# Kernel optimization log

Measured on AMD Instinct MI355X. Metric: run time of the kernel, lower is better.

Reference implementation:

```python
import jax, jax.numpy as jnp
import numpy as np

N = 100_000          # nodes
E = 3_200_000        # edges (avg degree 32)
H = 20               # hidden_channels (node feature width, = 10 one-hot + 10 mlp)
EH = 64              # edge_hidden_dim
EO = 10              # edge_output_dim
THRESHOLD = 1.0


def setup_inputs() -> dict:
    key = jax.random.key(0)
    ks = jax.random.split(key, 12)
    x = jax.random.normal(ks[0], (N, 2, H), dtype=jnp.float32)
    edge_index = jax.random.randint(ks[1], (2, E), 0, N, dtype=jnp.int32)
    # distances strictly in (0, threshold]
    edge_attr = jax.random.uniform(ks[2], (E, 1), jnp.float32, 1e-4, THRESHOLD)
    # parameters (torch.rand init as in the module)
    a = jax.random.uniform(ks[3], (1,), jnp.float32)
    b = jax.random.uniform(ks[4], (1,), jnp.float32) + 1.0
    gamma1 = jax.random.uniform(ks[5], (H, H), jnp.float32)
    gamma2 = jax.random.uniform(ks[6], (H, H), jnp.float32)
    bias = jax.random.uniform(ks[7], (H,), jnp.float32)
    # edge MLP: Linear(1, EH) -> ReLU -> Linear(EH, EO)
    W1 = jax.random.normal(ks[8], (1, EH), jnp.float32)
    b1 = jnp.zeros((EH,), jnp.float32)
    W2 = jax.random.normal(ks[9], (EH, EO), jnp.float32) / np.sqrt(EH)
    b2 = jnp.zeros((EO,), jnp.float32)
    return dict(x=x, edge_index=edge_index, edge_attr=edge_attr, a=a, b=b,
                gamma1=gamma1, gamma2=gamma2, bias=bias, W1=W1, b1=b1, W2=W2, b2=b2)


def reference(x, edge_index, edge_attr, a, b, gamma1, gamma2, bias, W1, b1, W2, b2):
    src, dst = edge_index[0], edge_index[1]
    # --- edge features ---
    h = jax.nn.relu(edge_attr @ W1 + b1)            # [E, EH]
    mlp_out = h @ W2 + b2                           # [E, EO]
    # one-hot distance bucket: 10 equal intervals over (0, threshold], idx 10 -> 9
    idx = jnp.clip((edge_attr[:, 0] * (10.0 / THRESHOLD)).astype(jnp.int32), 0, 9)
    one_hot = jax.nn.one_hot(idx, 10, dtype=x.dtype)  # [E, 10]
    eac = jnp.concatenate([one_hot, mlp_out], axis=1)  # edge_attr_combined [E, 20]
    # --- per-source-node normalization (w_tilde) ---
    sum_w = jax.ops.segment_sum(eac, src, num_segments=N)  # [N, 20]
    sw = sum_w[src]                                        # [E, 20]
    safe = jnp.where(sw != 0, sw, 1.0)
    w_tilde = jnp.where(sw != 0, eac / safe, jnp.asarray(0.01, x.dtype))
    # --- rho weighting on node features ---
    h_j = x[src, 0]                                  # [E, 20]
    h_jp = x[dst, 0]                                 # [E, 20]
    rho = jnp.abs(a * h_j - (1.0 - a) * h_jp) ** b   # [E, 20]
    # --- aggregate messages per source node ---
    sum_features = jax.ops.segment_sum(rho * w_tilde, src, num_segments=N)  # [N, 20]
    # --- node update ---
    out0 = jax.nn.sigmoid(x[:, 0] @ gamma1.T + sum_features @ gamma2.T + bias)
    return jnp.stack([out0, sum_features], axis=1)   # [N, 2, 20]
```

## Files before the change

kernel.cpp:

```cpp
#include <hip/hip_runtime.h>
#include <hip/hip_bf16.h>


#define BATCH 4096
#define BPT   16
#define BSH   7
#define CAP   4608
#define CAP8  640
#define GST   16

__device__ inline float blo(unsigned v) { return __uint_as_float(v << 16); }
__device__ inline float bhi(unsigned v) { return __uint_as_float(v & 0xFFFF0000u); }
__device__ inline unsigned f2bfu(float f) {
    __hip_bfloat16 h = __float2bfloat16(f);
    unsigned short us;
    __builtin_memcpy(&us, &h, 2);
    return (unsigned)us;
}

__device__ int block_scan_excl(int* data, int n, int* scratch) {
    const int t = threadIdx.x;
    const int lane = t & 63, w = t >> 6;
    const int base = t * 4;
    int v0 = (base + 0 < n) ? data[base + 0] : 0;
    int v1 = (base + 1 < n) ? data[base + 1] : 0;
    int v2 = (base + 2 < n) ? data[base + 2] : 0;
    int v3 = (base + 3 < n) ? data[base + 3] : 0;
    int p1 = v0 + v1, p2 = p1 + v2, p3 = p2 + v3;
    int x = p3;
    #pragma unroll
    for (int o = 1; o < 64; o <<= 1) { int y = __shfl_up(x, o); if (lane >= o) x += y; }
    if (lane == 63) scratch[w] = x;
    __syncthreads();
    int wbase = 0;
    for (int i = 0; i < w; ++i) wbase += scratch[i];
    int tb = wbase + x - p3;
    if (base + 0 < n) data[base + 0] = tb;
    if (base + 1 < n) data[base + 1] = tb + v0;
    if (base + 2 < n) data[base + 2] = tb + p1;
    if (base + 3 < n) data[base + 3] = tb + p2;
    int tot = scratch[0] + scratch[1] + scratch[2] + scratch[3];
    __syncthreads();
    return tot;
}

__launch_bounds__(256)
__global__ void k_scatter(const int* __restrict__ src, const int* __restrict__ dst,
                          const float* __restrict__ ea, int* __restrict__ gcursor,
                          int2* __restrict__ tmp,
                          const float* __restrict__ x, unsigned* __restrict__ xau,
                          const float* __restrict__ W1, const float* __restrict__ b1,
                          const float* __restrict__ W2, const float* __restrict__ b2,
                          float* __restrict__ AB, int* __restrict__ flag,
                          int E, int nb, int Npack, int EH, int EO) {
    __shared__ int2 pay2[BATCH];
    __shared__ int  lcount[1024];
    __shared__ int  lsave[1024];
    __shared__ int  scratch[4];
    const int t = threadIdx.x;
    const int xcd = blockIdx.x & 7;

    if (blockIdx.x == 0) {
        if (t == 64) {
            int ok = 1;
            for (int k = 0; k < EH; ++k) if (b1[k] != 0.0f) ok = 0;
            *flag = ok;
        }
        if (t < EO) {
            float A = 0.0f;
            for (int k = 0; k < EH; ++k)
                if (W1[k] > 0.0f) A = fmaf(W1[k], W2[k * EO + t], A);
            AB[t]      = A;
            AB[EO + t] = b2[t];
        }
    }

    for (int i = t; i < 1024; i += 256) lcount[i] = 0;
    __syncthreads();
    const int base = blockIdx.x * BATCH;
    int mys[BPT], myr[BPT], myw[BPT];
    #pragma unroll
    for (int k = 0; k < BPT; ++k) {
        int e = base + k * 256 + t;
        mys[k] = -1;
        if (e < E) {
            int s = src[e], d = dst[e];
            float dd = ea[e];
            int ib = (int)(dd * 10.0f);
            ib = ib < 0 ? 0 : (ib > 9 ? 9 : ib);
            int dq = (int)fmaf(dd, 2047.0f, 0.5f);
            dq = dq < 0 ? 0 : (dq > 2047 ? 2047 : dq);
            mys[k] = s;
            myr[k] = atomicAdd(&lcount[s >> BSH], 1);
            myw[k] = (d & 0x1FFFF) | (ib << 17) | (dq << 21);
        }
    }
    __syncthreads();
    for (int i = t; i < 1024; i += 256) lsave[i] = lcount[i];
    __syncthreads();
    int total = block_scan_excl(lcount, nb, scratch);
    for (int b = t; b < nb; b += 256) {
        int c = lsave[b];
        if (c > 0) lsave[b] = atomicAdd(&gcursor[(b * 8 + xcd) * GST], c);
    }
    __syncthreads();
    #pragma unroll
    for (int k = 0; k < BPT; ++k) {
        if (mys[k] >= 0) {
            int b = mys[k] >> BSH;
            int pos = lcount[b] + myr[k];
            pay2[pos] = make_int2(myw[k], (b << 7) | (mys[k] & 127));
        }
    }
    __syncthreads();
    for (int j = t; j < total; j += 256) {
        int2 v = pay2[j];
        int bb = v.y >> 7;
        int pos = lsave[bb] + (j - lcount[bb]);
        if (pos < CAP8) tmp[(size_t)(bb * 8 + xcd) * CAP8 + pos] = v;
    }
    const int stride = gridDim.x * 256;
    for (int i = blockIdx.x * 256 + t; i < Npack * 10; i += stride) {
        int n = i / 10, p = i - n * 10;
        float2 v = *(const float2*)(x + n * 40 + p * 2);
        xau[i] = f2bfu(v.x) | (f2bfu(v.y) << 16);
    }
}

template <int USE_XA>
__launch_bounds__(512, 8)
__global__ void k_nodeb(const float* __restrict__ x,
                        const unsigned* __restrict__ xau,
                        const int* __restrict__ gcount,
                        const int2* __restrict__ tmp,
                        const float* __restrict__ a_p, const float* __restrict__ b_p,
                        const float* __restrict__ g1, const float* __restrict__ g2,
                        const float* __restrict__ bias,
                        const float* __restrict__ AB, const int* __restrict__ flag_p,
                        const float* __restrict__ W1, const float* __restrict__ b1,
                        const float* __restrict__ W2, const float* __restrict__ b2,
                        float* __restrict__ out, int N, int EH, int EO) {
    __shared__ int   buf[CAP];
    __shared__ int   hist[128];
    __shared__ int   rowstart[129];
    __shared__ int   lcur[128];
    __shared__ unsigned char perm[128];
    __shared__ int   segm[8];
    __shared__ int   cps[9];
    __shared__ __hip_bfloat16 s_x0[128 * 22];
    __shared__ float s_sf[128 * 21];
    __shared__ float s_g1[20 * 21], s_g2[20 * 21], s_b[20];

    const int t = threadIdx.x;
    const int b = blockIdx.x;
    const int node0 = b << BSH;

    if (t < 128) hist[t] = 0;
    if (t < 64) {
        int c = (t < 8) ? gcount[(b * 8 + t) * GST] : 0;
        c = c > CAP8 ? CAP8 : c;
        int pr = (c + 1) >> 1;
        int acc = pr;
        #pragma unroll
        for (int o = 1; o < 8; o <<= 1) { int y = __shfl_up(acc, o); if (t >= o) acc += y; }
        if (t < 8) { segm[t] = c; cps[t] = acc - pr; }
        if (t == 7) cps[8] = acc;
    }
    for (int i = t; i < 400; i += 512) {
        int r = i / 20, cc = i - r * 20;
        s_g1[r * 21 + cc] = g1[i];
        s_g2[r * 21 + cc] = g2[i];
    }
    if (t < 20) s_b[t] = bias[t];
    if (USE_XA) {
        for (int i = t; i < 1280; i += 512) {
            int l = i / 10, p = i - l * 10;
            int n = node0 + l;
            unsigned v = (n < N) ? xau[n * 10 + p] : 0u;
            *(unsigned*)&s_x0[l * 22 + 2 * p] = v;
        }
    } else {
        for (int i = t; i < 2560; i += 512) {
            int l = i / 20, cc = i - l * 20;
            int n = node0 + l;
            s_x0[l * 22 + cc] = __float2bfloat16((n < N) ? x[n * 40 + cc] : 0.0f);
        }
    }
    __syncthreads();

    const int TP = cps[8];
    int vw[10], vn[10];
    #pragma unroll
    for (int k = 0; k < 5; ++k) {
        int pidx = k * 512 + t;
        vn[k * 2 + 0] = -1;
        vn[k * 2 + 1] = -1;
        if (pidx < TP) {
            int r = 0;
            #pragma unroll
            for (int rr = 1; rr < 8; ++rr) if (pidx >= cps[rr]) r = rr;
            int lp = pidx - cps[r];
            int mr = segm[r];
            const int4* sp = (const int4*)(tmp + (size_t)(b * 8 + r) * CAP8);
            int4 wv = sp[lp];
            int e0 = lp << 1;
            vw[k * 2 + 0] = wv.x;
            vw[k * 2 + 1] = wv.z;
            { vn[k * 2 + 0] = wv.y & 127; atomicAdd(&hist[vn[k * 2 + 0]], 1); }
            if (e0 + 1 < mr) { vn[k * 2 + 1] = wv.w & 127; atomicAdd(&hist[vn[k * 2 + 1]], 1); }
        }
    }
    __syncthreads();
    if (t < 64) {
        int a = hist[2 * t], bb = hist[2 * t + 1];
        int s = a + bb;
        int xsc = s;
        #pragma unroll
        for (int o = 1; o < 64; o <<= 1) { int y = __shfl_up(xsc, o); if (t >= o) xsc += y; }
        int excl = xsc - s;
        rowstart[2 * t]     = excl;
        rowstart[2 * t + 1] = excl + a;
        lcur[2 * t]         = excl;
        lcur[2 * t + 1]     = excl + a;
        if (t == 63) rowstart[128] = xsc;
    }
    __syncthreads();
    #pragma unroll
    for (int k = 0; k < 10; ++k) {
        if (vn[k] >= 0) {
            int p = atomicAdd(&lcur[vn[k]], 1);
            if (p < CAP) buf[p] = vw[k];
        }
    }
    __syncthreads();

    if (t < 128) hist[t] = 0;
    __syncthreads();
    if (t < 128) {
        int len = rowstart[t + 1] - rowstart[t];
        int bin = 127 - (len > 127 ? 127 : len);
        atomicAdd(&hist[bin], 1);
    }
    __syncthreads();
    if (t < 64) {
        int a = hist[2 * t], bb = hist[2 * t + 1];
        int s = a + bb;
        int xsc = s;
        #pragma unroll
        for (int o = 1; o < 64; o <<= 1) { int y = __shfl_up(xsc, o); if (t >= o) xsc += y; }
        int excl = xsc - s;
        hist[2 * t]     = excl;
        hist[2 * t + 1] = excl + a;
    }
    __syncthreads();
    if (t < 128) {
        int len = rowstart[t + 1] - rowstart[t];
        int bin = 127 - (len > 127 ? 127 : len);
        int pos = atomicAdd(&hist[bin], 1);
        perm[pos] = (unsigned char)t;
    }

    const float av = a_p[0], bv = b_p[0];
    const float am1 = 1.0f - av;
    const int fl = *flag_p;
    __syncthreads();

    const uint2* xg = (const uint2*)xau;
    #pragma unroll
    for (int r = 0; r < 2; ++r) {
        int item = t + 512 * r;
        if (item >= 640) break;
        int li = perm[item / 5];
        int q  = item - (item / 5) * 5;
        int c0 = q * 4;
        const bool cl0 = (c0 + 0) < 10, cl1 = (c0 + 1) < 10;
        const bool cl2 = (c0 + 2) < 10, cl3 = (c0 + 3) < 10;
        unsigned xv0 = *(const unsigned*)&s_x0[li * 22 + c0];
        unsigned xv1 = *(const unsigned*)&s_x0[li * 22 + c0 + 2];
        const float pax0 = av * blo(xv0), pax1 = av * bhi(xv0);
        const float pax2 = av * blo(xv1), pax3 = av * bhi(xv1);
        int rs = rowstart[li];
        int re = rowstart[li + 1];
        float deg = (float)(re - rs);
        float sf0, sf1, sf2, sf3;
        if (fl || (c0 + 3) < 10) {
            float sA0 = 0.f, sB0 = 0.f, s20 = 0.f;
            float sA1 = 0.f, sB1 = 0.f, s21 = 0.f;
            float sA2 = 0.f, sB2 = 0.f, s22 = 0.f;
            float sA3 = 0.f, sB3 = 0.f, s23 = 0.f;
            #pragma unroll 2
            for (int i = rs; i < re; ++i) {
                int w = buf[i];
                float xd0, xd1, xd2, xd3;
                if (USE_XA) {
                    uint2 v = xg[(unsigned)(w & 0x1FFFF) * 5u + (unsigned)q];
                    xd0 = blo(v.x); xd1 = bhi(v.x);
                    xd2 = blo(v.y); xd3 = bhi(v.y);
                } else {
                    int n = w & 0x1FFFF;
                    xd0 = x[n * 40 + c0];     xd1 = x[n * 40 + c0 + 1];
                    xd2 = x[n * 40 + c0 + 2]; xd3 = x[n * 40 + c0 + 3];
                }
                int   ib  = (w >> 17) & 0xF;
                float dqf = (float)(((unsigned)w) >> 21);
                float r0 = exp2f(bv * __log2f(fabsf(fmaf(-am1, xd0, pax0))));
                float r1 = exp2f(bv * __log2f(fabsf(fmaf(-am1, xd1, pax1))));
                float r2 = exp2f(bv * __log2f(fabsf(fmaf(-am1, xd2, pax2))));
                float r3 = exp2f(bv * __log2f(fabsf(fmaf(-am1, xd3, pax3))));
                float e0s = cl0 ? ((ib == c0)     ? 1.0f : 0.0f) : dqf;
                float e1s = cl1 ? ((ib == c0 + 1) ? 1.0f : 0.0f) : dqf;
                float e2s = cl2 ? ((ib == c0 + 2) ? 1.0f : 0.0f) : dqf;
                float e3s = cl3 ? ((ib == c0 + 3) ? 1.0f : 0.0f) : dqf;
                sA0 += e0s; sB0 = fmaf(r0, e0s, sB0); s20 += r0;
                sA1 += e1s; sB1 = fmaf(r1, e1s, sB1); s21 += r1;
                sA2 += e2s; sB2 = fmaf(r2, e2s, sB2); s22 += r2;
                sA3 += e3s; sB3 = fmaf(r3, e3s, sB3); s23 += r3;
            }
            #define FIN(K, sAk, sBk, s2k, sfk)                                     \
            {   int ck = c0 + K;                                                   \
                float sw, s1;                                                      \
                if (ck < 10) { sw = sAk; s1 = sBk; }                               \
                else { float Afq = AB[ck - 10] * (1.0f / 2047.0f);                 \
                       float Bf  = AB[ck];                                         \
                       sw = fmaf(Afq, sAk, Bf * deg);                              \
                       s1 = fmaf(Afq, sBk, Bf * s2k); }                            \
                sfk = (sw != 0.0f) ? (s1 / sw) : (0.01f * s2k);                    \
            }
            FIN(0, sA0, sB0, s20, sf0); FIN(1, sA1, sB1, s21, sf1);
            FIN(2, sA2, sB2, s22, sf2); FIN(3, sA3, sB3, s23, sf3);
            #undef FIN
        } else {
            float swk[4] = {0.f, 0.f, 0.f, 0.f};
            float s1k[4] = {0.f, 0.f, 0.f, 0.f};
            float s2k[4] = {0.f, 0.f, 0.f, 0.f};
            float paxs[4] = {pax0, pax1, pax2, pax3};
            for (int i = rs; i < re; ++i) {
                int w = buf[i];
                float xd[4];
                if (USE_XA) {
                    uint2 v = xg[(unsigned)(w & 0x1FFFF) * 5u + (unsigned)q];
                    xd[0] = blo(v.x); xd[1] = bhi(v.x);
                    xd[2] = blo(v.y); xd[3] = bhi(v.y);
                } else {
                    int n = w & 0x1FFFF;
                    #pragma unroll
                    for (int kk = 0; kk < 4; ++kk) xd[kk] = x[n * 40 + c0 + kk];
                }
                int   ib  = (w >> 17) & 0xF;
                float dd_ = (float)(((unsigned)w) >> 21) * (1.0f / 2047.0f);
                float mlp[4];
                #pragma unroll
                for (int kk = 0; kk < 4; ++kk) {
                    int ck = c0 + kk;
                    mlp[kk] = b2[ck >= 10 ? ck - 10 : 0];
                }
                for (int k_ = 0; k_ < EH; ++k_) {
                    float h_ = fmaf(dd_, W1[k_], b1[k_]);
                    h_ = h_ > 0.0f ? h_ : 0.0f;
                    #pragma unroll
                    for (int kk = 0; kk < 4; ++kk) {
                        int ck = c0 + kk;
                        mlp[kk] = fmaf(h_, W2[k_ * EO + (ck >= 10 ? ck - 10 : 0)], mlp[kk]);
                    }
                }
                #pragma unroll
                for (int kk = 0; kk < 4; ++kk) {
                    int ck = c0 + kk;
                    float rho = exp2f(bv * __log2f(fabsf(fmaf(-am1, xd[kk], paxs[kk]))));
                    float sel = (ck < 10) ? ((ib == ck) ? 1.0f : 0.0f) : mlp[kk];
                    swk[kk] += sel;
                    s1k[kk] = fmaf(rho, sel, s1k[kk]);
                    s2k[kk] += rho;
                }
            }
            sf0 = (swk[0] != 0.0f) ? (s1k[0] / swk[0]) : (0.01f * s2k[0]);
            sf1 = (swk[1] != 0.0f) ? (s1k[1] / swk[1]) : (0.01f * s2k[1]);
            sf2 = (swk[2] != 0.0f) ? (s1k[2] / swk[2]) : (0.01f * s2k[2]);
            sf3 = (swk[3] != 0.0f) ? (s1k[3] / swk[3]) : (0.01f * s2k[3]);
        }
        s_sf[li * 21 + c0]     = sf0;
        s_sf[li * 21 + c0 + 1] = sf1;
        s_sf[li * 21 + c0 + 2] = sf2;
        s_sf[li * 21 + c0 + 3] = sf3;
    }
    __syncthreads();

    for (int i = t; i < 2560; i += 512) {
        int l = i / 20, cc = i - l * 20;
        int n = node0 + l;
        if (n < N) {
            float acc = s_b[cc];
            const __hip_bfloat16* xr = &s_x0[l * 22];
            const float* sr  = &s_sf[l * 21];
            const float* g1r = &s_g1[cc * 21];
            const float* g2r = &s_g2[cc * 21];
            #pragma unroll
            for (int k = 0; k < 20; ++k)
                acc = fmaf(__bfloat162float(xr[k]), g1r[k], fmaf(sr[k], g2r[k], acc));
            float o0 = 1.0f / (1.0f + __expf(-acc));
            out[n * 40 + cc]      = o0;
            out[n * 40 + 20 + cc] = sr[cc];
        }
    }
}

extern "C" void kernel_launch(void* const* d_in, const int* in_sizes, int n_in,
                              void* d_out, int out_size, void* d_ws, size_t ws_size,
                              hipStream_t stream) {
    const float* x    = (const float*)d_in[0];
    const int*   ei   = (const int*)  d_in[1];
    const float* ea   = (const float*)d_in[2];
    const float* a_p  = (const float*)d_in[3];
    const float* b_p  = (const float*)d_in[4];
    const float* g1   = (const float*)d_in[5];
    const float* g2   = (const float*)d_in[6];
    const float* bias = (const float*)d_in[7];
    const float* W1   = (const float*)d_in[8];
    const float* b1   = (const float*)d_in[9];
    const float* W2   = (const float*)d_in[10];
    const float* b2   = (const float*)d_in[11];
    float* out = (float*)d_out;

    const int E  = in_sizes[2];
    const int N  = in_sizes[0] / 40;
    const int EH = in_sizes[8];
    const int EO = in_sizes[11];
    const int* src = ei;
    const int* dst = ei + E;

    const int nb     = (N + 127) >> BSH;
    const int nbatch = (E + BATCH - 1) / BATCH;

    char* wsb = (char*)d_ws;
    size_t o = 0;
    int* gcursor = (int*)(wsb + o); o += (size_t)nb * 8 * GST * 4;
    float* AB    = (float*)(wsb + o); o += 2 * (size_t)EO * 4;
    int* flag    = (int*)(wsb + o);   o += 4;                   o = (o + 15) & ~(size_t)15;
    int2* tmp    = (int2*)(wsb + o);  o += (size_t)nb * 8 * CAP8 * 8;
    unsigned* xau = (unsigned*)(wsb + o);
    const size_t need_xa = o + (size_t)N * 10 * 4;
    const int use_xa = (ws_size >= need_xa) ? 1 : 0;

    hipMemsetAsync(gcursor, 0, (size_t)nb * 8 * GST * sizeof(int), stream);

    k_scatter<<<nbatch, 256, 0, stream>>>(src, dst, ea, gcursor, tmp,
                                          x, use_xa ? xau : (unsigned*)AB,
                                          W1, b1, W2, b2, AB, flag,
                                          E, nb, use_xa ? N : 0, EH, EO);
    if (use_xa) {
        k_nodeb<1><<<nb, 512, 0, stream>>>(x, xau, gcursor, tmp, a_p, b_p,
                                           g1, g2, bias, AB, flag,
                                           W1, b1, W2, b2, out, N, EH, EO);
    } else {
        k_nodeb<0><<<nb, 512, 0, stream>>>(x, xau, gcursor, tmp, a_p, b_p,
                                           g1, g2, bias, AB, flag,
                                           W1, b1, W2, b2, out, N, EH, EO);
    }
}
```

Baseline: 225.6 us.

## Split node-bucket kernel into two half-blocks of 64 nodes each

The node aggregation kernel now launches two 320-thread blocks per 128-node bucket. Each block reads every edge in the bucket but keeps only those whose local node falls in its half, which shrinks shared-memory buffers and per-block work so more blocks can be resident. The scatter batch size and per-thread count are also halved. In exchange, each bucket's edge records are read twice, and the smaller CAPH buffer could drop edges if one half holds more than its capacity.

```diff
diff --git a/kernel.cpp b/kernel.cpp
--- a/kernel.cpp
+++ b/kernel.cpp
@@ -2,10 +2,10 @@
 #include <hip/hip_bf16.h>
 
 
-#define BATCH 4096
-#define BPT   16
+#define BATCH 2048
+#define BPT   8
 #define BSH   7
-#define CAP   4608
+#define CAPH  2560
 #define CAP8  640
 #define GST   16
 
@@ -128,34 +128,35 @@
 }
 
 template <int USE_XA>
-__launch_bounds__(512, 8)
-__global__ void k_nodeb(const float* __restrict__ x,
-                        const unsigned* __restrict__ xau,
-                        const int* __restrict__ gcount,
-                        const int2* __restrict__ tmp,
-                        const float* __restrict__ a_p, const float* __restrict__ b_p,
-                        const float* __restrict__ g1, const float* __restrict__ g2,
-                        const float* __restrict__ bias,
-                        const float* __restrict__ AB, const int* __restrict__ flag_p,
-                        const float* __restrict__ W1, const float* __restrict__ b1,
-                        const float* __restrict__ W2, const float* __restrict__ b2,
-                        float* __restrict__ out, int N, int EH, int EO) {
-    __shared__ int   buf[CAP];
-    __shared__ int   hist[128];
-    __shared__ int   rowstart[129];
-    __shared__ int   lcur[128];
-    __shared__ unsigned char perm[128];
+__launch_bounds__(320, 6)
+__global__ void k_nodebh(const float* __restrict__ x,
+                         const unsigned* __restrict__ xau,
+                         const int* __restrict__ gcount,
+                         const int2* __restrict__ tmp,
+                         const float* __restrict__ a_p, const float* __restrict__ b_p,
+                         const float* __restrict__ g1, const float* __restrict__ g2,
+                         const float* __restrict__ bias,
+                         const float* __restrict__ AB, const int* __restrict__ flag_p,
+                         const float* __restrict__ W1, const float* __restrict__ b1,
+                         const float* __restrict__ W2, const float* __restrict__ b2,
+                         float* __restrict__ out, int N, int EH, int EO) {
+    __shared__ int   buf[CAPH];
+    __shared__ int   hist[64];
+    __shared__ int   rowstart[65];
+    __shared__ int   lcur[64];
+    __shared__ unsigned char perm[64];
     __shared__ int   segm[8];
     __shared__ int   cps[9];
-    __shared__ __hip_bfloat16 s_x0[128 * 22];
-    __shared__ float s_sf[128 * 21];
+    __shared__ __hip_bfloat16 s_x0[64 * 22];
+    __shared__ float s_sf[64 * 21];
     __shared__ float s_g1[20 * 21], s_g2[20 * 21], s_b[20];
 
     const int t = threadIdx.x;
-    const int b = blockIdx.x;
-    const int node0 = b << BSH;
-
-    if (t < 128) hist[t] = 0;
+    const int b = blockIdx.x >> 1;
+    const int h = blockIdx.x & 1;
+    const int node0 = (b << BSH) + (h << 6);
+
+    if (t < 64) hist[t] = 0;
     if (t < 64) {
         int c = (t < 8) ? gcount[(b * 8 + t) * GST] : 0;
         c = c > CAP8 ? CAP8 : c;
@@ -166,21 +167,21 @@
         if (t < 8) { segm[t] = c; cps[t] = acc - pr; }
         if (t == 7) cps[8] = acc;
     }
-    for (int i = t; i < 400; i += 512) {
+    for (int i = t; i < 400; i += 320) {
         int r = i / 20, cc = i - r * 20;
         s_g1[r * 21 + cc] = g1[i];
         s_g2[r * 21 + cc] = g2[i];
     }
     if (t < 20) s_b[t] = bias[t];
     if (USE_XA) {
-        for (int i = t; i < 1280; i += 512) {
+        for (int i = t; i < 640; i += 320) {
             int l = i / 10, p = i - l * 10;
             int n = node0 + l;
             unsigned v = (n < N) ? xau[n * 10 + p] : 0u;
             *(unsigned*)&s_x0[l * 22 + 2 * p] = v;
         }
     } else {
-        for (int i = t; i < 2560; i += 512) {
+        for (int i = t; i < 1280; i += 320) {
             int l = i / 20, cc = i - l * 20;
             int n = node0 + l;
             s_x0[l * 22 + cc] = __float2bfloat16((n < N) ? x[n * 40 + cc] : 0.0f);
@@ -189,10 +190,10 @@
     __syncthreads();
 
     const int TP = cps[8];
-    int vw[10], vn[10];
+    int vw[16], vn[16];
     #pragma unroll
-    for (int k = 0; k < 5; ++k) {
-        int pidx = k * 512 + t;
+    for (int k = 0; k < 8; ++k) {
+        int pidx = k * 320 + t;
         vn[k * 2 + 0] = -1;
         vn[k * 2 + 1] = -1;
         if (pidx < TP) {
@@ -204,58 +205,62 @@
             const int4* sp = (const int4*)(tmp + (size_t)(b * 8 + r) * CAP8);
             int4 wv = sp[lp];
             int e0 = lp << 1;
-            vw[k * 2 + 0] = wv.x;
-            vw[k * 2 + 1] = wv.z;
-            { vn[k * 2 + 0] = wv.y & 127; atomicAdd(&hist[vn[k * 2 + 0]], 1); }
-            if (e0 + 1 < mr) { vn[k * 2 + 1] = wv.w & 127; atomicAdd(&hist[vn[k * 2 + 1]], 1); }
+            int n0 = wv.y & 127;
+            if ((n0 >> 6) == h) {
+                vw[k * 2 + 0] = wv.x;
+                vn[k * 2 + 0] = n0 & 63;
+                atomicAdd(&hist[n0 & 63], 1);
+            }
+            if (e0 + 1 < mr) {
+                int n1 = wv.w & 127;
+                if ((n1 >> 6) == h) {
+                    vw[k * 2 + 1] = wv.z;
+                    vn[k * 2 + 1] = n1 & 63;
+                    atomicAdd(&hist[n1 & 63], 1);
+                }
+            }
         }
     }
     __syncthreads();
     if (t < 64) {
-        int a = hist[2 * t], bb = hist[2 * t + 1];
-        int s = a + bb;
+        int s = hist[t];
         int xsc = s;
         #pragma unroll
         for (int o = 1; o < 64; o <<= 1) { int y = __shfl_up(xsc, o); if (t >= o) xsc += y; }
         int excl = xsc - s;
-        rowstart[2 * t]     = excl;
-        rowstart[2 * t + 1] = excl + a;
-        lcur[2 * t]         = excl;
-        lcur[2 * t + 1]     = excl + a;
-        if (t == 63) rowstart[128] = xsc;
+        rowstart[t] = excl;
+        lcur[t]     = excl;
+        if (t == 63) rowstart[64] = xsc;
     }
     __syncthreads();
     #pragma unroll
-    for (int k = 0; k < 10; ++k) {
+    for (int k = 0; k < 16; ++k) {
         if (vn[k] >= 0) {
             int p = atomicAdd(&lcur[vn[k]], 1);
-            if (p < CAP) buf[p] = vw[k];
-        }
-    }
-    __syncthreads();
-
-    if (t < 128) hist[t] = 0;
-    __syncthreads();
-    if (t < 128) {
+            if (p < CAPH) buf[p] = vw[k];
+        }
+    }
+    __syncthreads();
+
+    if (t < 64) hist[t] = 0;
+    __syncthreads();
+    if (t < 64) {
         int len = rowstart[t + 1] - rowstart[t];
-        int bin = 127 - (len > 127 ? 127 : len);
+        int bin = 63 - (len > 63 ? 63 : len);
         atomicAdd(&hist[bin], 1);
     }
     __syncthreads();
     if (t < 64) {
-        int a = hist[2 * t], bb = hist[2 * t + 1];
-        int s = a + bb;
+        int s = hist[t];
         int xsc = s;
         #pragma unroll
         for (int o = 1; o < 64; o <<= 1) { int y = __shfl_up(xsc, o); if (t >= o) xsc += y; }
-        int excl = xsc - s;
-        hist[2 * t]     = excl;
-        hist[2 * t + 1] = excl + a;
-    }
-    __syncthreads();
-    if (t < 128) {
+        hist[t] = xsc - s;
+    }
+    __syncthreads();
+    if (t < 64) {
         int len = rowstart[t + 1] - rowstart[t];
-        int bin = 127 - (len > 127 ? 127 : len);
+        int bin = 63 - (len > 63 ? 63 : len);
         int pos = atomicAdd(&hist[bin], 1);
         perm[pos] = (unsigned char)t;
     }
@@ -266,10 +271,8 @@
     __syncthreads();
 
     const uint2* xg = (const uint2*)xau;
-    #pragma unroll
-    for (int r = 0; r < 2; ++r) {
-        int item = t + 512 * r;
-        if (item >= 640) break;
+    {
+        int item = t;
         int li = perm[item / 5];
         int q  = item - (item / 5) * 5;
         int c0 = q * 4;
@@ -385,7 +388,7 @@
     }
     __syncthreads();
 
-    for (int i = t; i < 2560; i += 512) {
+    for (int i = t; i < 1280; i += 320) {
         int l = i / 20, cc = i - l * 20;
         int n = node0 + l;
         if (n < N) {
@@ -448,12 +451,12 @@
                                           W1, b1, W2, b2, AB, flag,
                                           E, nb, use_xa ? N : 0, EH, EO);
     if (use_xa) {
-        k_nodeb<1><<<nb, 512, 0, stream>>>(x, xau, gcursor, tmp, a_p, b_p,
-                                           g1, g2, bias, AB, flag,
-                                           W1, b1, W2, b2, out, N, EH, EO);
+        k_nodebh<1><<<nb * 2, 320, 0, stream>>>(x, xau, gcursor, tmp, a_p, b_p,
+                                                g1, g2, bias, AB, flag,
+                                                W1, b1, W2, b2, out, N, EH, EO);
     } else {
-        k_nodeb<0><<<nb, 512, 0, stream>>>(x, xau, gcursor, tmp, a_p, b_p,
-                                           g1, g2, bias, AB, flag,
-                                           W1, b1, W2, b2, out, N, EH, EO);
+        k_nodebh<0><<<nb * 2, 320, 0, stream>>>(x, xau, gcursor, tmp, a_p, b_p,
+                                                g1, g2, bias, AB, flag,
+                                                W1, b1, W2, b2, out, N, EH, EO);
     }
 }
```

After: 241.3 us. 7.0% more time.
